# Kernel tuning notes

Measured on AMD Instinct MI355X. Metric: run time of the kernel, lower is better.

Reference implementation:

```python
import jax, jax.numpy as jnp
import numpy as np
from math import sqrt

# Dims: B batch, L frames, N points/frame, DIM transformer dim,
# J joints, M memory slots per joint, FD final_dim = DIM//8, OUT = 3*J
B, L, N, DIM = 4, 24, 512, 1024
J, M, FD, OUT = 24, 64, 128, 72


def setup_inputs() -> dict:
    key = jax.random.key(0)
    ks = jax.random.split(key, 8)
    w = lambda k, shape: jax.random.normal(k, shape, jnp.float32) * 0.02
    return {
        "feat": jax.random.normal(ks[0], (B, L, N, DIM), jnp.float32),
        "seg_w": w(ks[1], (J, DIM)),
        "seg_b": jnp.zeros((J,), jnp.float32),
        "pc_w": w(ks[2], (FD, DIM)),
        "pc_b": jnp.zeros((FD,), jnp.float32),
        "mem": jax.random.normal(ks[3], (FD, J * M), jnp.float32),
        "ln_g": jnp.ones((FD,), jnp.float32),
        "ln_b": jnp.zeros((FD,), jnp.float32),
        "w1": w(ks[4], (FD // 2, FD)),
        "b1": jnp.zeros((FD // 2,), jnp.float32),
        "w2": w(ks[5], (OUT, FD // 2)),
        "b2": jnp.zeros((OUT,), jnp.float32),
    }


def forward_mem(y, s, mem):
    # y: (B, Nt, D) point features; s: (B, Nt, J) seg weights; mem: (D, J*M)
    Bn, Nt, D = y.shape
    # affinity of every token to every (joint, slot) memory entry
    logits = jnp.einsum('dk,bnd->bkn', mem, y) / sqrt(D)            # (B, J*M, Nt)
    # per-joint segmentation weighting of the logits
    logits = logits.reshape(Bn, J, M, Nt) * s.transpose(0, 2, 1)[:, :, None, :]
    attn = jax.nn.softmax(logits.reshape(Bn, J * M, Nt), axis=1)     # over memory slots
    return jnp.einsum('dk,bkn->bnd', mem, attn)                      # (B, Nt, D)


def reference(feat, seg_w, seg_b, pc_w, pc_b, mem, ln_g, ln_b, w1, b1, w2, b2):
    Bn, Lf, Np, C = feat.shape
    # seg_head: 1x1 conv == per-point linear -> softmax over joints
    seg = jnp.einsum('blnc,jc->blnj', feat, seg_w) + seg_b           # (B,L,N,J)
    seg = jax.nn.softmax(seg.reshape(Bn, Lf * Np, J), axis=-1)       # (B, L*N, J)
    seg_out = seg.reshape(Bn, Lf, Np, J).transpose(0, 1, 3, 2)       # (B,L,J,N)
    # pc_head: per-point projection to final_dim
    pc = (jnp.einsum('blnc,fc->blnf', feat, pc_w) + pc_b).reshape(Bn, Lf * Np, FD)
    rec = forward_mem(pc, seg, mem)                                  # (B, L*N, FD)
    loss_rec = jnp.mean((rec - pc) ** 2)
    skl = jnp.max(rec, axis=1)                                       # (B, FD)
    # skl_head: LayerNorm -> Linear -> GELU -> Linear
    mu = jnp.mean(skl, axis=-1, keepdims=True)
    var = jnp.var(skl, axis=-1, keepdims=True)
    h = (skl - mu) * jax.lax.rsqrt(var + 1e-5) * ln_g + ln_b
    h = jax.nn.gelu(h @ w1.T + b1, approximate=False)
    skl_out = h @ w2.T + b2                                          # (B, OUT)
    return skl_out, seg_out, loss_rec
```

## Files before the change

### kernel.cpp

```cpp
#include <hip/hip_runtime.h>

typedef __bf16 bf16_t;
typedef bf16_t bf16x8 __attribute__((ext_vector_type(8)));
typedef float f32x4 __attribute__((ext_vector_type(4)));
typedef unsigned short u16;

#define MFMA16 __builtin_amdgcn_mfma_f32_16x16x32_bf16

#define NT_TOK   12288
#define T_TOK    49152

#define WS_PC    0
#define WS_S     25165824
#define WS_WP    29884416
#define WS_MTP   30212096
#define WS_MFP   30605312
#define WS_SKL   30998528
#define WS_LOSS  31000576

__device__ __forceinline__ u16 f2bf(float f) {
  union { bf16_t h; u16 u; } c; c.h = (bf16_t)f; return c.u;
}

__device__ __forceinline__ void atomic_max_f32(float* a, float v) {
  if (v >= 0.f) atomicMax((int*)a, __float_as_int(v));
  else atomicMin((unsigned int*)a, (unsigned int)__float_as_int(v));
}

#define GLD16(g, l) __builtin_amdgcn_global_load_lds( \
    (const __attribute__((address_space(1))) void*)(g), \
    (__attribute__((address_space(3))) void*)(l), 16, 0, 0)

__global__ void k_init(const float* __restrict__ seg_w, const float* __restrict__ pc_w,
                       const float* __restrict__ mem,
                       u16* __restrict__ Wp, u16* __restrict__ mTp, u16* __restrict__ mFp,
                       float* __restrict__ skl, float* __restrict__ loss)
{
  int i = blockIdx.x * 256 + threadIdx.x;
  union { u16 s[8]; uint4 v; } u;
  if (i < 20480) {
    int lane = i & 63, blk = i >> 6;
    int kc = blk / 10, t = blk - kc * 10;
    int n = lane & 15, q = lane >> 4;
    int row = t * 16 + n;
    int k0 = kc * 32 + q * 8;
    #pragma unroll
    for (int e = 0; e < 8; ++e) {
      float v = 0.f;
      if (row < 24) v = seg_w[row * 1024 + k0 + e];
      else if (row < 152) v = pc_w[(row - 24) * 1024 + k0 + e];
      u.s[e] = f2bf(v);
    }
    *(uint4*)(Wp + (size_t)i * 8) = u.v;
  } else if ((i -= 20480) < 24576) {
    int lane = i & 63, blk = i >> 6;
    int j = blk >> 4, rem = blk & 15, wv = rem >> 2, ks = rem & 3;
    int n = lane & 15, q = lane >> 4;
    int slot = j * 64 + wv * 16 + n;
    int d0 = ks * 32 + q * 8;
    #pragma unroll
    for (int e = 0; e < 8; ++e)
      u.s[e] = f2bf(mem[(size_t)(d0 + e) * 1536 + slot]);
    *(uint4*)(mTp + (size_t)i * 8) = u.v;
  } else if ((i -= 24576) < 24576) {
    int lane = i & 63, blk = i >> 6;
    int j = blk >> 4, h = (blk >> 3) & 1, wv = (blk >> 1) & 3, ft = blk & 1;
    int n = lane & 15, q = lane >> 4;
    int f = wv * 32 + ft * 16 + n;
    int s0 = j * 64 + h * 32 + q * 8;
    #pragma unroll
    for (int e = 0; e < 8; ++e)
      u.s[e] = f2bf(mem[(size_t)f * 1536 + s0 + e]);
    *(uint4*)(mFp + (size_t)i * 8) = u.v;
  } else if ((i -= 24576) < 512) {
    skl[i] = -__builtin_inff();
  } else if (i == 512) {
    *loss = 0.f;
  }
}

__global__ __launch_bounds__(256, 3) void k_proj(
    const float* __restrict__ feat, const u16* __restrict__ Wp,
    const float* __restrict__ seg_b, const float* __restrict__ pc_b,
    float* __restrict__ pc_out, float* __restrict__ s_out, float* __restrict__ out_seg)
{
  __shared__ __align__(16) u16 wbuf[2][10240];

  const int tid = threadIdx.x;
  const int w = tid >> 6;
  const int lane = tid & 63;
  const int n = lane & 15;
  const int q = lane >> 4;
  const int base = blockIdx.x * 64;

  f32x4 acc[10];
  #pragma unroll
  for (int t = 0; t < 10; ++t) acc[t] = (f32x4){0.f, 0.f, 0.f, 0.f};

  const float* fp0 = feat + (size_t)(base + w * 16 + n) * 1024 + q * 8;

  {
    const u16* gW = Wp;
    #pragma unroll
    for (int i = 0; i < 5; ++i) {
      const int off = i * 2048 + w * 512;
      GLD16(gW + off + lane * 8, &wbuf[0][off]);
    }
  }
  float4 fcur[2][2], fnext[2][2];
  #pragma unroll
  for (int kc2 = 0; kc2 < 2; ++kc2) {
    const float4* a = (const float4*)(fp0 + kc2 * 32);
    fcur[kc2][0] = a[0];
    fcur[kc2][1] = a[1];
  }
  __syncthreads();

  for (int c = 0; c < 16; ++c) {
    const u16* lb = &wbuf[c & 1][0];

    if (c < 15) {
      const u16* gW = Wp + (size_t)(c + 1) * 10240;
      u16* nb = &wbuf[(c + 1) & 1][0];
      #pragma unroll
      for (int i = 0; i < 5; ++i) {
        const int off = i * 2048 + w * 512;
        GLD16(gW + off + lane * 8, nb + off);
      }
      #pragma unroll
      for (int kc2 = 0; kc2 < 2; ++kc2) {
        const float4* a = (const float4*)(fp0 + ((c + 1) * 2 + kc2) * 32);
        fnext[kc2][0] = a[0];
        fnext[kc2][1] = a[1];
      }
    }

    #pragma unroll
    for (int kc2 = 0; kc2 < 2; ++kc2) {
      bf16x8 bw[10];
      #pragma unroll
      for (int t = 0; t < 10; ++t)
        bw[t] = *(const bf16x8*)(lb + (size_t)(kc2 * 10 + t) * 512 + lane * 8);
      float4 x0 = fcur[kc2][0], y0 = fcur[kc2][1];
      bf16x8 af;
      af[0] = (bf16_t)x0.x; af[1] = (bf16_t)x0.y; af[2] = (bf16_t)x0.z; af[3] = (bf16_t)x0.w;
      af[4] = (bf16_t)y0.x; af[5] = (bf16_t)y0.y; af[6] = (bf16_t)y0.z; af[7] = (bf16_t)y0.w;
      #pragma unroll
      for (int t = 0; t < 10; ++t)
        acc[t] = MFMA16(af, bw[t], acc[t], 0, 0, 0);
    }

    __syncthreads();

    #pragma unroll
    for (int kc2 = 0; kc2 < 2; ++kc2) {
      fcur[kc2][0] = fnext[kc2][0];
      fcur[kc2][1] = fnext[kc2][1];
    }
  }

  #pragma unroll
  for (int r = 0; r < 4; ++r) {
    const int token = base + w * 16 + q * 4 + r;
    float v0 = acc[0][r] + seg_b[n];
    float v1 = (n < 8) ? (acc[1][r] + seg_b[16 + n]) : -__builtin_inff();
    float mx = fmaxf(v0, v1);
    #pragma unroll
    for (int d2 = 1; d2 < 16; d2 <<= 1) mx = fmaxf(mx, __shfl_xor(mx, d2, 16));
    float e0 = __expf(v0 - mx);
    float e1 = (n < 8) ? __expf(v1 - mx) : 0.f;
    float sm = e0 + e1;
    #pragma unroll
    for (int d2 = 1; d2 < 16; d2 <<= 1) sm += __shfl_xor(sm, d2, 16);
    float is = 1.f / sm;
    float s0v = e0 * is, s1v = e1 * is;
    s_out[(size_t)token * 24 + n] = s0v;
    if (n < 8) s_out[(size_t)token * 24 + 16 + n] = s1v;
    const int b = token / NT_TOK;
    const int rem = token - b * NT_TOK;
    const int l = rem >> 9, p = rem & 511;
    float* so = out_seg + ((size_t)(b * 24 + l) * 24) * 512 + p;
    so[(size_t)n * 512] = s0v;
    if (n < 8) so[(size_t)(16 + n) * 512] = s1v;
    #pragma unroll
    for (int t = 1; t < 10; ++t) {
      int col = t * 16 + n;
      if (col >= 24 && col < 152) {
        pc_out[(size_t)token * 128 + (col - 24)] = acc[t][r] + pc_b[col - 24];
      }
    }
  }
}

#define AS_S     0
#define AS_P     6656
#define AS_LW    15872
#define AS_RL    16896
#define AS_TOT   16912

__global__ __launch_bounds__(256, 3) void k_attn(
    const float* __restrict__ pc, const float* __restrict__ s_in,
    const u16* __restrict__ mFp, const u16* __restrict__ mTp,
    float* __restrict__ skl, float* __restrict__ loss)
{
  __shared__ __align__(16) char smem[AS_TOT];
  float* s_tile = (float*)(smem + AS_S);
  u16* Pl  = (u16*)(smem + AS_P);
  float* lw  = (float*)(smem + AS_LW);
  float* redL = (float*)(smem + AS_RL);

  const int tid = threadIdx.x;
  const int w = tid >> 6, lane = tid & 63, n = lane & 15, q = lane >> 4;
  const int base = blockIdx.x * 64;

  for (int i = tid; i < 1536; i += 256) {
    int t = i / 24, jj = i - t * 24;
    s_tile[t * 26 + jj] = s_in[(size_t)base * 24 + i];
  }

  bf16x8 qf[4][4];
  #pragma unroll
  for (int tt = 0; tt < 4; ++tt)
    #pragma unroll
    for (int ks = 0; ks < 4; ++ks) {
      const float4* qp = (const float4*)(pc + (size_t)(base + tt * 16 + n) * 128 + ks * 32 + q * 8);
      float4 x = qp[0], y = qp[1];
      bf16x8 a;
      a[0] = (bf16_t)x.x; a[1] = (bf16_t)x.y; a[2] = (bf16_t)x.z; a[3] = (bf16_t)x.w;
      a[4] = (bf16_t)y.x; a[5] = (bf16_t)y.y; a[6] = (bf16_t)y.z; a[7] = (bf16_t)y.w;
      qf[tt][ks] = a;
    }

  f32x4 o[4][2];
  #pragma unroll
  for (int tt = 0; tt < 4; ++tt) {
    o[tt][0] = (f32x4){0.f, 0.f, 0.f, 0.f};
    o[tt][1] = (f32x4){0.f, 0.f, 0.f, 0.f};
  }
  float l_acc[4] = {0.f, 0.f, 0.f, 0.f};

  const u16* mT_frag = mTp + (size_t)(w * 4) * 512 + lane * 8;
  const u16* mF_frag = mFp + (size_t)(w * 2) * 512 + lane * 8;

  const float invs = 0.088388347648318447f;
  __syncthreads();

  for (int j = 0; j < 24; ++j) {
    f32x4 sacc[4];
    #pragma unroll
    for (int tt = 0; tt < 4; ++tt) sacc[tt] = (f32x4){0.f, 0.f, 0.f, 0.f};
    #pragma unroll
    for (int ks = 0; ks < 4; ++ks) {
      bf16x8 am = *(const bf16x8*)(mT_frag + (size_t)(j * 16 + ks) * 512);
      #pragma unroll
      for (int tt = 0; tt < 4; ++tt)
        sacc[tt] = MFMA16(am, qf[tt][ks], sacc[tt], 0, 0, 0);
    }

    __syncthreads();
    #pragma unroll
    for (int tt = 0; tt < 4; ++tt) {
      float sj = s_tile[(tt * 16 + n) * 26 + j] * invs;
      float p0 = __expf(sacc[tt][0] * sj);
      float p1 = __expf(sacc[tt][1] * sj);
      float p2 = __expf(sacc[tt][2] * sj);
      float p3 = __expf(sacc[tt][3] * sj);
      l_acc[tt] += (p0 + p1) + (p2 + p3);
      ushort4 pk;
      pk.x = f2bf(p0); pk.y = f2bf(p1); pk.z = f2bf(p2); pk.w = f2bf(p3);
      *(ushort4*)(&Pl[(tt * 16 + n) * 72 + w * 16 + q * 4]) = pk;
    }
    __syncthreads();

    #pragma unroll
    for (int h = 0; h < 2; ++h) {
      bf16x8 bm[2];
      #pragma unroll
      for (int ft = 0; ft < 2; ++ft)
        bm[ft] = *(const bf16x8*)(mF_frag + (size_t)(j * 16 + h * 8 + ft) * 512);
      #pragma unroll
      for (int tt = 0; tt < 4; ++tt) {
        bf16x8 pa = *(const bf16x8*)(&Pl[(tt * 16 + n) * 72 + h * 32 + q * 8]);
        o[tt][0] = MFMA16(pa, bm[0], o[tt][0], 0, 0, 0);
        o[tt][1] = MFMA16(pa, bm[1], o[tt][1], 0, 0, 0);
      }
    }
  }

  #pragma unroll
  for (int tt = 0; tt < 4; ++tt) {
    float v = l_acc[tt];
    v += __shfl_xor(v, 16, 64);
    v += __shfl_xor(v, 32, 64);
    if (q == 0) lw[w * 64 + tt * 16 + n] = v;
  }
  __syncthreads();

  float lsum = 0.f;
  float fmax2[2] = {-__builtin_inff(), -__builtin_inff()};
  #pragma unroll
  for (int tt = 0; tt < 4; ++tt) {
    f32x4 linv;
    #pragma unroll
    for (int r = 0; r < 4; ++r) {
      int tok = tt * 16 + q * 4 + r;
      float lt = lw[tok] + lw[64 + tok] + lw[128 + tok] + lw[192 + tok];
      linv[r] = 1.f / lt;
    }
    #pragma unroll
    for (int ft = 0; ft < 2; ++ft)
      #pragma unroll
      for (int r = 0; r < 4; ++r) {
        const int token = base + tt * 16 + q * 4 + r;
        const int f = w * 32 + ft * 16 + n;
        float rec = o[tt][ft][r] * linv[r];
        float d = rec - pc[(size_t)token * 128 + f];
        lsum += d * d;
        fmax2[ft] = fmaxf(fmax2[ft], rec);
      }
  }
  #pragma unroll
  for (int ft = 0; ft < 2; ++ft) {
    float v = fmax2[ft];
    v = fmaxf(v, __shfl_xor(v, 16, 64));
    v = fmaxf(v, __shfl_xor(v, 32, 64));
    if (q == 0) atomic_max_f32(&skl[(base / NT_TOK) * 128 + w * 32 + ft * 16 + n], v);
  }
  #pragma unroll
  for (int d2 = 1; d2 < 64; d2 <<= 1) lsum += __shfl_xor(lsum, d2, 64);
  if (lane == 0) redL[w] = lsum;
  __syncthreads();
  if (tid == 0) atomicAdd(loss, redL[0] + redL[1] + redL[2] + redL[3]);
}

__global__ void k_head(const float* __restrict__ skl,
                       const float* __restrict__ ln_g, const float* __restrict__ ln_b,
                       const float* __restrict__ w1, const float* __restrict__ b1,
                       const float* __restrict__ w2, const float* __restrict__ b2,
                       const float* __restrict__ loss, float* __restrict__ out)
{
  __shared__ float hbuf[128];
  __shared__ float gbuf[64];
  __shared__ float red[4];
  const int t = threadIdx.x;
  const int ln = t & 63, wv = t >> 6;
  for (int b = 0; b < 4; ++b) {
    float x = skl[b * 128 + t];
    float s1 = x, s2 = x * x;
    #pragma unroll
    for (int d = 1; d < 64; d <<= 1) {
      s1 += __shfl_xor(s1, d, 64);
      s2 += __shfl_xor(s2, d, 64);
    }
    if (ln == 0) { red[wv * 2] = s1; red[wv * 2 + 1] = s2; }
    __syncthreads();
    float mu = (red[0] + red[2]) * (1.f / 128.f);
    float var = (red[1] + red[3]) * (1.f / 128.f) - mu * mu;
    float hn = (x - mu) * rsqrtf(var + 1e-5f) * ln_g[t] + ln_b[t];
    hbuf[t] = hn;
    __syncthreads();
    if (t < 64) {
      float a = b1[t];
      for (int c = 0; c < 128; ++c) a += hbuf[c] * w1[t * 128 + c];
      gbuf[t] = 0.5f * a * (1.f + erff(a * 0.70710678118654752f));
    }
    __syncthreads();
    if (t < 72) {
      float a = b2[t];
      for (int c = 0; c < 64; ++c) a += gbuf[c] * w2[t * 64 + c];
      out[b * 72 + t] = a;
    }
    __syncthreads();
  }
  if (t == 0) out[1179936] = loss[0] * (1.f / 6291456.f);
}

extern "C" void kernel_launch(void* const* d_in, const int* in_sizes, int n_in,
                              void* d_out, int out_size, void* d_ws, size_t ws_size,
                              hipStream_t stream) {
  (void)in_sizes; (void)n_in; (void)out_size; (void)ws_size;
  const float* feat  = (const float*)d_in[0];
  const float* seg_w = (const float*)d_in[1];
  const float* seg_b = (const float*)d_in[2];
  const float* pc_w  = (const float*)d_in[3];
  const float* pc_b  = (const float*)d_in[4];
  const float* mem   = (const float*)d_in[5];
  const float* ln_g  = (const float*)d_in[6];
  const float* ln_b  = (const float*)d_in[7];
  const float* w1    = (const float*)d_in[8];
  const float* b1    = (const float*)d_in[9];
  const float* w2    = (const float*)d_in[10];
  const float* b2    = (const float*)d_in[11];

  char* ws = (char*)d_ws;
  float* pc_buf = (float*)(ws + WS_PC);
  float* s_buf  = (float*)(ws + WS_S);
  u16*   Wp     = (u16*)(ws + WS_WP);
  u16*   mTp    = (u16*)(ws + WS_MTP);
  u16*   mFp    = (u16*)(ws + WS_MFP);
  float* sklb   = (float*)(ws + WS_SKL);
  float* lossb  = (float*)(ws + WS_LOSS);
  float* out    = (float*)d_out;

  k_init<<<275, 256, 0, stream>>>(seg_w, pc_w, mem, Wp, mTp, mFp, sklb, lossb);
  k_proj<<<768, 256, 0, stream>>>(feat, Wp, seg_b, pc_b, pc_buf, s_buf, out + 288);
  k_attn<<<768, 256, 0, stream>>>(pc_buf, s_buf, mFp, mTp, sklb, lossb);
  k_head<<<1, 128, 0, stream>>>(sklb, ln_g, ln_b, w1, b1, w2, b2, lossb, out);
}
```

Baseline: 397.6 us.

## Deepen prefetch pipelines in projection GEMM and memory-attention loop

In the projection kernel, feature loads become a three-deep register ring buffer that prefetches two chunks ahead. The full __syncthreads is replaced by explicit vmcnt waits plus s_barrier and sched_barrier, so outstanding global loads can keep overlapping with the MFMAs. In the memory-attention kernel, the next joint's memory-key fragments and the current joint's value fragments are loaded before the synchronization and softmax phase, hiding global-load latency. The cost is more register pressure, and correctness now depends on hand-counted vmcnt values.

```diff
diff --git a/kernel.cpp b/kernel.cpp
--- a/kernel.cpp
+++ b/kernel.cpp
@@ -99,26 +99,27 @@
 
   const float* fp0 = feat + (size_t)(base + w * 16 + n) * 1024 + q * 8;
 
-  {
-    const u16* gW = Wp;
-    #pragma unroll
-    for (int i = 0; i < 5; ++i) {
-      const int off = i * 2048 + w * 512;
-      GLD16(gW + off + lane * 8, &wbuf[0][off]);
-    }
-  }
-  float4 fcur[2][2], fnext[2][2];
-  #pragma unroll
-  for (int kc2 = 0; kc2 < 2; ++kc2) {
-    const float4* a = (const float4*)(fp0 + kc2 * 32);
-    fcur[kc2][0] = a[0];
-    fcur[kc2][1] = a[1];
-  }
-  __syncthreads();
-
+  #pragma unroll
+  for (int i = 0; i < 5; ++i) {
+    const int off = i * 2048 + w * 512;
+    GLD16(Wp + off + lane * 8, &wbuf[0][off]);
+  }
+  __builtin_amdgcn_sched_barrier(0);
+  float4 fb[3][2][2];
+  #pragma unroll
+  for (int cc = 0; cc < 2; ++cc)
+    #pragma unroll
+    for (int kc2 = 0; kc2 < 2; ++kc2) {
+      const float4* a = (const float4*)(fp0 + (cc * 2 + kc2) * 32);
+      fb[cc][kc2][0] = a[0];
+      fb[cc][kc2][1] = a[1];
+    }
+  asm volatile("s_waitcnt vmcnt(8)");
+  __builtin_amdgcn_s_barrier();
+  __builtin_amdgcn_sched_barrier(0);
+
+  #pragma unroll
   for (int c = 0; c < 16; ++c) {
-    const u16* lb = &wbuf[c & 1][0];
-
     if (c < 15) {
       const u16* gW = Wp + (size_t)(c + 1) * 10240;
       u16* nb = &wbuf[(c + 1) & 1][0];
@@ -127,21 +128,25 @@
         const int off = i * 2048 + w * 512;
         GLD16(gW + off + lane * 8, nb + off);
       }
+      __builtin_amdgcn_sched_barrier(0);
+    }
+    if (c < 14) {
       #pragma unroll
       for (int kc2 = 0; kc2 < 2; ++kc2) {
-        const float4* a = (const float4*)(fp0 + ((c + 1) * 2 + kc2) * 32);
-        fnext[kc2][0] = a[0];
-        fnext[kc2][1] = a[1];
+        const float4* a = (const float4*)(fp0 + ((c + 2) * 2 + kc2) * 32);
+        fb[(c + 2) % 3][kc2][0] = a[0];
+        fb[(c + 2) % 3][kc2][1] = a[1];
       }
     }
 
+    const u16* lb = &wbuf[c & 1][0];
     #pragma unroll
     for (int kc2 = 0; kc2 < 2; ++kc2) {
       bf16x8 bw[10];
       #pragma unroll
       for (int t = 0; t < 10; ++t)
         bw[t] = *(const bf16x8*)(lb + (size_t)(kc2 * 10 + t) * 512 + lane * 8);
-      float4 x0 = fcur[kc2][0], y0 = fcur[kc2][1];
+      float4 x0 = fb[c % 3][kc2][0], y0 = fb[c % 3][kc2][1];
       bf16x8 af;
       af[0] = (bf16_t)x0.x; af[1] = (bf16_t)x0.y; af[2] = (bf16_t)x0.z; af[3] = (bf16_t)x0.w;
       af[4] = (bf16_t)y0.x; af[5] = (bf16_t)y0.y; af[6] = (bf16_t)y0.z; af[7] = (bf16_t)y0.w;
@@ -150,12 +155,11 @@
         acc[t] = MFMA16(af, bw[t], acc[t], 0, 0, 0);
     }
 
-    __syncthreads();
-
-    #pragma unroll
-    for (int kc2 = 0; kc2 < 2; ++kc2) {
-      fcur[kc2][0] = fnext[kc2][0];
-      fcur[kc2][1] = fnext[kc2][1];
+    if (c < 15) {
+      if (c < 14) asm volatile("s_waitcnt vmcnt(4)");
+      else        asm volatile("s_waitcnt vmcnt(0)");
+      __builtin_amdgcn_s_barrier();
+      __builtin_amdgcn_sched_barrier(0);
     }
   }
 
@@ -243,18 +247,35 @@
   const u16* mF_frag = mFp + (size_t)(w * 2) * 512 + lane * 8;
 
   const float invs = 0.088388347648318447f;
+
+  bf16x8 amc[4];
+  #pragma unroll
+  for (int ks = 0; ks < 4; ++ks)
+    amc[ks] = *(const bf16x8*)(mT_frag + (size_t)ks * 512);
+
   __syncthreads();
 
   for (int j = 0; j < 24; ++j) {
+    bf16x8 bm[4];
+    #pragma unroll
+    for (int hf = 0; hf < 4; ++hf)
+      bm[hf] = *(const bf16x8*)(mF_frag + (size_t)(j * 16 + (hf >> 1) * 8 + (hf & 1)) * 512);
+
     f32x4 sacc[4];
     #pragma unroll
     for (int tt = 0; tt < 4; ++tt) sacc[tt] = (f32x4){0.f, 0.f, 0.f, 0.f};
     #pragma unroll
     for (int ks = 0; ks < 4; ++ks) {
-      bf16x8 am = *(const bf16x8*)(mT_frag + (size_t)(j * 16 + ks) * 512);
       #pragma unroll
       for (int tt = 0; tt < 4; ++tt)
-        sacc[tt] = MFMA16(am, qf[tt][ks], sacc[tt], 0, 0, 0);
+        sacc[tt] = MFMA16(amc[ks], qf[tt][ks], sacc[tt], 0, 0, 0);
+    }
+
+    bf16x8 amn[4];
+    if (j < 23) {
+      #pragma unroll
+      for (int ks = 0; ks < 4; ++ks)
+        amn[ks] = *(const bf16x8*)(mT_frag + (size_t)((j + 1) * 16 + ks) * 512);
     }
 
     __syncthreads();
@@ -273,18 +294,17 @@
     __syncthreads();
 
     #pragma unroll
-    for (int h = 0; h < 2; ++h) {
-      bf16x8 bm[2];
-      #pragma unroll
-      for (int ft = 0; ft < 2; ++ft)
-        bm[ft] = *(const bf16x8*)(mF_frag + (size_t)(j * 16 + h * 8 + ft) * 512);
-      #pragma unroll
-      for (int tt = 0; tt < 4; ++tt) {
-        bf16x8 pa = *(const bf16x8*)(&Pl[(tt * 16 + n) * 72 + h * 32 + q * 8]);
-        o[tt][0] = MFMA16(pa, bm[0], o[tt][0], 0, 0, 0);
-        o[tt][1] = MFMA16(pa, bm[1], o[tt][1], 0, 0, 0);
-      }
-    }
+    for (int tt = 0; tt < 4; ++tt) {
+      bf16x8 pa0 = *(const bf16x8*)(&Pl[(tt * 16 + n) * 72 + q * 8]);
+      o[tt][0] = MFMA16(pa0, bm[0], o[tt][0], 0, 0, 0);
+      o[tt][1] = MFMA16(pa0, bm[1], o[tt][1], 0, 0, 0);
+      bf16x8 pa1 = *(const bf16x8*)(&Pl[(tt * 16 + n) * 72 + 32 + q * 8]);
+      o[tt][0] = MFMA16(pa1, bm[2], o[tt][0], 0, 0, 0);
+      o[tt][1] = MFMA16(pa1, bm[3], o[tt][1], 0, 0, 0);
+    }
+
+    #pragma unroll
+    for (int ks = 0; ks < 4; ++ks) amc[ks] = amn[ks];
   }
 
   #pragma unroll
```

After: 393.5 us. About the same (-1.0%).
